# Kernel tuning notes

Hardware: AMD Instinct MI355X
Metric: run time of the kernel (lower is better)

## Reference

```python
import jax, jax.numpy as jnp
import numpy as np

ALPHA = 0.2   # leaky relu negative slope
EPS = 1e-5    # layernorm eps
NEG = -1e12   # mask value from original code


def gat_layer(x, adj, W, a):
    # x: [N, F_in], adj: [N, N] bool, W: [F_in, F_out], a: [2*F_out, 1]
    F_out = W.shape[1]
    Wh = x @ W                                  # [N, F_out]
    # a^T [Wh_i ; Wh_j] decomposes into f1_i + f2_j (same math as the
    # O(N^2 * 2F) concat in the torch code, without materializing it)
    f1 = Wh @ a[:F_out]                         # [N, 1]
    f2 = Wh @ a[F_out:]                         # [N, 1]
    e = jax.nn.leaky_relu(f1 + f2.T, negative_slope=ALPHA)  # [N, N]
    att = jnp.where(adj, e, NEG)
    att = jax.nn.softmax(att, axis=1)           # dropout p=0.0 -> no-op
    return att @ Wh                             # [N, F_out]


def layernorm(x, g, b):
    mu = jnp.mean(x, axis=-1, keepdims=True)
    var = jnp.var(x, axis=-1, keepdims=True)
    return (x - mu) * jax.lax.rsqrt(var + EPS) * g + b


def setup_inputs() -> dict:
    N, F = 8192, 128
    key = jax.random.key(0)
    ks = jax.random.split(key, 12)
    inp = {
        "input_hs": jax.random.normal(ks[0], (2, N, F), jnp.float32),
        "adjs": jax.random.uniform(ks[1], (2, N, N)) < 0.3,   # bool adjacency
        "MPNN_emb": jax.random.normal(ks[2], (N, F), jnp.float32),
        "query": jax.random.normal(ks[3], (1, F), jnp.float32),
        # learned params (xavier-ish scale)
        "W0": jax.random.normal(ks[4], (F, F), jnp.float32) * (1.414 / np.sqrt(F)),
        "a0": jax.random.normal(ks[5], (2 * F, 1), jnp.float32) * 0.1,
        "W1": jax.random.normal(ks[6], (F, F), jnp.float32) * (1.414 / np.sqrt(F)),
        "a1": jax.random.normal(ks[7], (2 * F, 1), jnp.float32) * 0.1,
        "ln_gamma": jnp.ones((F,), jnp.float32),
        "ln_beta": jnp.zeros((F,), jnp.float32),
        "res": jax.random.normal(ks[8], (1, 1), jnp.float32) * 0.5,
    }
    return inp


def reference(input_hs, adjs, MPNN_emb, query, W0, a0, W1, a1, ln_gamma, ln_beta, res):
    h0 = gat_layer(input_hs[0], adjs[0], W0, a0)   # [N, F]
    h1 = gat_layer(input_hs[1], adjs[1], W1, a1)   # [N, F]
    q = layernorm(query, ln_gamma, ln_beta)        # [1, F]
    w1 = q @ h0.T                                  # [1, N]
    w2 = q @ h1.T
    w3 = q @ MPNN_emb.T
    scores = jax.nn.softmax(jnp.concatenate([w1, w2, w3], axis=0), axis=0)  # [3, N]
    # diag_embed(s) @ H is just per-row scaling s[:, None] * H
    mix = (scores[0][:, None] * h0
           + scores[1][:, None] * h1
           + scores[2][:, None] * MPNN_emb)
    return res * mix + input_hs[0]
```

## Files before the change

kernel.cpp:

```cpp
#include <hip/hip_runtime.h>
#include <hip/hip_bf16.h>
#include <cstdint>


#define N 8192
#define F 128
#define JS 8

typedef __attribute__((ext_vector_type(8))) short short8;
typedef __attribute__((ext_vector_type(8))) unsigned short ushort8;
typedef __attribute__((ext_vector_type(4))) float floatx4;

__device__ inline unsigned int f2bf(float x) {
  unsigned int u = __float_as_uint(x);
  u += 0x7FFFu + ((u >> 16) & 1u);
  return u >> 16;
}


__global__ __launch_bounds__(128) void k1_wh(
    const float* __restrict__ X2, const float* __restrict__ W0,
    const float* __restrict__ W1, const float* __restrict__ a0,
    const float* __restrict__ a1, unsigned short* __restrict__ Whbt,
    float* __restrict__ f1g, float* __restrict__ f2g) {
  const int l  = blockIdx.y;
  const int i0 = blockIdx.x * 16;
  const int c  = threadIdx.x;
  const float* __restrict__ X = X2 + (size_t)l * N * F + (size_t)i0 * F;
  const float* __restrict__ W = l ? W1 : W0;

  __shared__ __align__(16) float sX[16 * F];
  __shared__ float red[2][2][16];
  {
    const float4* src = (const float4*)X;
    float4* dst = (float4*)sX;
#pragma unroll
    for (int qq = 0; qq < 4; ++qq) dst[qq * 128 + c] = src[qq * 128 + c];
  }
  __syncthreads();

  float acc[16];
#pragma unroll
  for (int r = 0; r < 16; ++r) acc[r] = 0.f;

  for (int f4 = 0; f4 < 32; ++f4) {
    float w0 = W[(f4 * 4 + 0) * F + c];
    float w1 = W[(f4 * 4 + 1) * F + c];
    float w2 = W[(f4 * 4 + 2) * F + c];
    float w3 = W[(f4 * 4 + 3) * F + c];
#pragma unroll
    for (int r = 0; r < 16; ++r) {
      float4 xv = *(const float4*)(&sX[r * F + f4 * 4]);
      acc[r] = fmaf(xv.x, w0, acc[r]);
      acc[r] = fmaf(xv.y, w1, acc[r]);
      acc[r] = fmaf(xv.z, w2, acc[r]);
      acc[r] = fmaf(xv.w, w3, acc[r]);
    }
  }

  {
    unsigned short* wdst = Whbt + (size_t)l * F * N + (size_t)c * N + i0;
    ushort8 u0, u1;
#pragma unroll
    for (int r = 0; r < 8; ++r) {
      u0[r] = (unsigned short)f2bf(acc[r]);
      u1[r] = (unsigned short)f2bf(acc[8 + r]);
    }
    *(ushort8*)wdst = u0;
    *(ushort8*)(wdst + 8) = u1;
  }

  const float* __restrict__ a = l ? a1 : a0;
  const float a1c = a[c], a2c = a[F + c];
  const int w = c >> 6, lane = c & 63;
#pragma unroll
  for (int r = 0; r < 16; ++r) {
    float s1 = acc[r] * a1c;
    float s2 = acc[r] * a2c;
#pragma unroll
    for (int off = 32; off; off >>= 1) {
      s1 += __shfl_down(s1, off);
      s2 += __shfl_down(s2, off);
    }
    if (lane == 0) {
      red[w][0][r] = s1;
      red[w][1][r] = s2;
    }
  }
  __syncthreads();
  if (c < 16)
    f1g[l * N + i0 + c] = red[0][0][c] + red[1][0][c];
  else if (c < 32)
    f2g[l * N + i0 + c - 16] = red[0][1][c - 16] + red[1][1][c - 16];
}

__global__ __launch_bounds__(128) void k3_qln(
    const float* __restrict__ query, const float* __restrict__ gamma,
    const float* __restrict__ beta, float* __restrict__ qln) {
  const int t = threadIdx.x;
  float v = query[t];
  float s = v, sq = v * v;
#pragma unroll
  for (int off = 32; off; off >>= 1) {
    s += __shfl_down(s, off);
    sq += __shfl_down(sq, off);
  }
  __shared__ float sb[4];
  if ((t & 63) == 0) {
    sb[t >> 6] = s;
    sb[2 + (t >> 6)] = sq;
  }
  __syncthreads();
  float S = sb[0] + sb[1], SQ = sb[2] + sb[3];
  float mu = S * (1.f / 128.f);
  float var = SQ * (1.f / 128.f) - mu * mu;
  qln[t] = (v - mu) * rsqrtf(var + 1e-5f) * gamma[t] + beta[t];
}

__device__ inline short8 make_pfrag(float f1v, const float4& fa,
                                    const float4& fb, const int4& a0,
                                    const int4& a1, float& Lacc) {
  float p0, p1, p2, p3, p4, p5, p6, p7, sc;
  sc = f1v + fa.x; sc = fmaxf(sc, 0.2f * sc); p0 = a0.x ? __expf(sc) : 0.f;
  sc = f1v + fa.y; sc = fmaxf(sc, 0.2f * sc); p1 = a0.y ? __expf(sc) : 0.f;
  sc = f1v + fa.z; sc = fmaxf(sc, 0.2f * sc); p2 = a0.z ? __expf(sc) : 0.f;
  sc = f1v + fa.w; sc = fmaxf(sc, 0.2f * sc); p3 = a0.w ? __expf(sc) : 0.f;
  sc = f1v + fb.x; sc = fmaxf(sc, 0.2f * sc); p4 = a1.x ? __expf(sc) : 0.f;
  sc = f1v + fb.y; sc = fmaxf(sc, 0.2f * sc); p5 = a1.y ? __expf(sc) : 0.f;
  sc = f1v + fb.z; sc = fmaxf(sc, 0.2f * sc); p6 = a1.z ? __expf(sc) : 0.f;
  sc = f1v + fb.w; sc = fmaxf(sc, 0.2f * sc); p7 = a1.w ? __expf(sc) : 0.f;
  Lacc += ((p0 + p1) + (p2 + p3)) + ((p4 + p5) + (p6 + p7));
  union { unsigned int u[4]; short8 s8; } r;
  r.u[0] = f2bf(p0) | (f2bf(p1) << 16);
  r.u[1] = f2bf(p2) | (f2bf(p3) << 16);
  r.u[2] = f2bf(p4) | (f2bf(p5) << 16);
  r.u[3] = f2bf(p6) | (f2bf(p7) << 16);
  return r.s8;
}

__global__ __launch_bounds__(256) void k2_attn(
    const unsigned short* __restrict__ Whbt, const float* __restrict__ f1g,
    const float* __restrict__ f2g, const int* __restrict__ adj,
    float* __restrict__ hpart, float* __restrict__ Lpart) {
  const int l  = blockIdx.y;
  const int s  = blockIdx.z;
  const int i0 = blockIdx.x * 128;
  const int t  = threadIdx.x;
  const int wave = t >> 6, lane = t & 63;
  const int lpos = lane & 15, halfk = lane >> 4;

  __shared__ __align__(16) unsigned short sB[128][136];

  const unsigned short* __restrict__ WhbL = Whbt + (size_t)l * F * N;
  const int* __restrict__ adjL = adj + (size_t)l * N * N;
  const float* __restrict__ f2L = f2g + l * N;

  const int rowA = i0 + wave * 32 + lpos;
  const float f1a = f1g[l * N + rowA];
  const float f1b = f1g[l * N + rowA + 16];
  const int* __restrict__ adjA = adjL + (size_t)rowA * N + halfk * 8;
  const int* __restrict__ adjB = adjA + (size_t)16 * N;
  const float* __restrict__ f2base = f2L + halfk * 8;

  const unsigned short* __restrict__ wsrc = WhbL + (size_t)(t >> 1) * N + (t & 1) * 8;
  unsigned short* __restrict__ sdst = &sB[t >> 1][(t & 1) * 8];

  floatx4 acc[2][8];
#pragma unroll
  for (int mt = 0; mt < 2; ++mt)
#pragma unroll
    for (int nt = 0; nt < 8; ++nt) acc[mt][nt] = (floatx4){0.f, 0.f, 0.f, 0.f};
  float Lacc0 = 0.f, Lacc1 = 0.f;

  const int jbeg = s * (N / JS);

  int4 ca0 = *(const int4*)(adjA + jbeg);
  int4 ca1 = *(const int4*)(adjA + jbeg + 4);
  int4 cb0 = *(const int4*)(adjB + jbeg);
  int4 cb1 = *(const int4*)(adjB + jbeg + 4);

  for (int st = 0; st < (N / JS) / 128; ++st) {
    const int jb = jbeg + st * 128;
    __syncthreads();
#pragma unroll
    for (int r = 0; r < 8; ++r)
      *(uint4*)(sdst + r * 16) = *(const uint4*)(wsrc + jb + r * 16);
    __syncthreads();

#pragma unroll
    for (int s4 = 0; s4 < 4; ++s4) {
      const int j0 = jb + s4 * 32;
      int jn = j0 + 32;
      if (jn >= jbeg + (N / JS)) jn = jbeg;
      int4 na0 = *(const int4*)(adjA + jn);
      int4 na1 = *(const int4*)(adjA + jn + 4);
      int4 nb0 = *(const int4*)(adjB + jn);
      int4 nb1 = *(const int4*)(adjB + jn + 4);
      float4 fa = *(const float4*)(f2base + j0);
      float4 fb = *(const float4*)(f2base + j0 + 4);

      short8 af0 = make_pfrag(f1a, fa, fb, ca0, ca1, Lacc0);
      short8 af1 = make_pfrag(f1b, fa, fb, cb0, cb1, Lacc1);

      const unsigned short* bp = &sB[lpos][s4 * 32 + halfk * 8];
#pragma unroll
      for (int nt = 0; nt < 8; ++nt) {
        short8 bf = *(const short8*)(bp + nt * 16 * 136);
        acc[0][nt] = __builtin_amdgcn_mfma_f32_16x16x32_bf16(af0, bf, acc[0][nt], 0, 0, 0);
        acc[1][nt] = __builtin_amdgcn_mfma_f32_16x16x32_bf16(af1, bf, acc[1][nt], 0, 0, 0);
      }
      ca0 = na0; ca1 = na1; cb0 = nb0; cb1 = nb1;
    }
  }

  const size_t obase = ((size_t)(l * JS + s) * N + i0) * F;
  const size_t lbase = (size_t)(l * JS + s) * N + i0;
#pragma unroll
  for (int mt = 0; mt < 2; ++mt) {
    const int rb = wave * 32 + mt * 16 + halfk * 4;
#pragma unroll
    for (int nt = 0; nt < 8; ++nt) {
#pragma unroll
      for (int reg = 0; reg < 4; ++reg)
        hpart[obase + (size_t)(rb + reg) * F + nt * 16 + lpos] = acc[mt][nt][reg];
    }
  }
  Lacc0 += __shfl_xor(Lacc0, 16);
  Lacc0 += __shfl_xor(Lacc0, 32);
  Lacc1 += __shfl_xor(Lacc1, 16);
  Lacc1 += __shfl_xor(Lacc1, 32);
  if (halfk == 0) {
    Lpart[lbase + wave * 32 + lpos] = Lacc0;
    Lpart[lbase + wave * 32 + 16 + lpos] = Lacc1;
  }
}

__global__ __launch_bounds__(256) void k4_mix(
    const float* __restrict__ hpart, const float* __restrict__ Lpart,
    const float* __restrict__ MPNN, const float* __restrict__ qln,
    const float* __restrict__ x0, const float* __restrict__ res,
    float* __restrict__ out) {
  const int row  = blockIdx.x * 4 + (threadIdx.x >> 6);
  const int lane = threadIdx.x & 63;
  const int c    = lane * 2;

  float h0x = 0.f, h0y = 0.f, h1x = 0.f, h1y = 0.f, L0 = 0.f, L1 = 0.f;
#pragma unroll
  for (int sx = 0; sx < JS; ++sx) {
    float2 v0 = *(const float2*)&hpart[((size_t)(0 * JS + sx) * N + row) * F + c];
    float2 v1 = *(const float2*)&hpart[((size_t)(1 * JS + sx) * N + row) * F + c];
    h0x += v0.x; h0y += v0.y;
    h1x += v1.x; h1y += v1.y;
    L0 += Lpart[(size_t)(0 * JS + sx) * N + row];
    L1 += Lpart[(size_t)(1 * JS + sx) * N + row];
  }
  const float i0v = 1.f / L0, i1v = 1.f / L1;
  h0x *= i0v; h0y *= i0v;
  h1x *= i1v; h1y *= i1v;

  float2 mv = *(const float2*)&MPNN[(size_t)row * F + c];
  float2 qv = *(const float2*)&qln[c];
  float w1 = qv.x * h0x + qv.y * h0y;
  float w2 = qv.x * h1x + qv.y * h1y;
  float w3 = qv.x * mv.x + qv.y * mv.y;
#pragma unroll
  for (int off = 1; off < 64; off <<= 1) {
    w1 += __shfl_xor(w1, off);
    w2 += __shfl_xor(w2, off);
    w3 += __shfl_xor(w3, off);
  }
  float m = fmaxf(w1, fmaxf(w2, w3));
  float e1 = __expf(w1 - m), e2 = __expf(w2 - m), e3 = __expf(w3 - m);
  float inv = res[0] / (e1 + e2 + e3);
  float2 xr = *(const float2*)&x0[(size_t)row * F + c];
  float2 o;
  o.x = (e1 * h0x + e2 * h1x + e3 * mv.x) * inv + xr.x;
  o.y = (e1 * h0y + e2 * h1y + e3 * mv.y) * inv + xr.y;
  *(float2*)&out[(size_t)row * F + c] = o;
}

extern "C" void kernel_launch(void* const* d_in, const int* in_sizes, int n_in,
                              void* d_out, int out_size, void* d_ws,
                              size_t ws_size, hipStream_t stream) {
  const float* x2    = (const float*)d_in[0];
  const int*   adj   = (const int*)d_in[1];
  const float* mpnn  = (const float*)d_in[2];
  const float* query = (const float*)d_in[3];
  const float* W0    = (const float*)d_in[4];
  const float* a0    = (const float*)d_in[5];
  const float* W1    = (const float*)d_in[6];
  const float* a1    = (const float*)d_in[7];
  const float* gamma = (const float*)d_in[8];
  const float* beta  = (const float*)d_in[9];
  const float* res   = (const float*)d_in[10];

  float* ws = (float*)d_ws;
  unsigned short* Whbt = (unsigned short*)ws;
  float* hpart = ws + 1048576;
  float* f1g   = ws + 17825792;
  float* f2g   = ws + 17842176;
  float* Lpart = ws + 17858560;
  float* qln   = ws + 17989632;
  float* out   = (float*)d_out;

  k1_wh<<<dim3(N / 16, 2), 128, 0, stream>>>(x2, W0, W1, a0, a1, Whbt, f1g, f2g);
  k3_qln<<<1, 128, 0, stream>>>(query, gamma, beta, qln);
  k2_attn<<<dim3(N / 128, 2, JS), 256, 0, stream>>>(Whbt, f1g, f2g, adj, hpart,
                                                    Lpart);
  k4_mix<<<N / 4, 256, 0, stream>>>(hpart, Lpart, mpnn, qln, x2, res, out);
}
```

Measured before the change: 816.5 us.

## Pre-pack adjacency into bitmasks and truncate bf16 conversion in attention kernel

Adds a streaming pre-pass kernel that packs the int32 adjacency matrix into 32-bit bitmasks. The attention kernel then reads one uint4 of mask bits per 128-column stage instead of prefetching int4 adjacency vectors for every 32-column step. The intent is to move the bulk adjacency read into a simple coalesced streaming kernel and shrink the load pressure and registers inside the MFMA loop. The cost is one extra launch plus a 16 MB mask written and read back. Separately, the float-to-bf16 conversion of the attention probabilities now truncates instead of rounding to nearest even, which saves ALU work but adds a small precision loss.

```diff
diff --git a/kernel.cpp b/kernel.cpp
--- a/kernel.cpp
+++ b/kernel.cpp
@@ -17,6 +17,22 @@
   return u >> 16;
 }
 
+
+__global__ __launch_bounds__(256) void k0_pack(const int* __restrict__ adj,
+                                               unsigned int* __restrict__ mask) {
+  const size_t gid = (size_t)blockIdx.x * 256 + threadIdx.x;
+  const int4* p = (const int4*)adj + gid * 8;
+  unsigned int m = 0;
+#pragma unroll
+  for (int q = 0; q < 8; ++q) {
+    int4 v = p[q];
+    m |= (v.x != 0) ? (1u << (q * 4 + 0)) : 0u;
+    m |= (v.y != 0) ? (1u << (q * 4 + 1)) : 0u;
+    m |= (v.z != 0) ? (1u << (q * 4 + 2)) : 0u;
+    m |= (v.w != 0) ? (1u << (q * 4 + 3)) : 0u;
+  }
+  mask[gid] = m;
+}
 
 __global__ __launch_bounds__(128) void k1_wh(
     const float* __restrict__ X2, const float* __restrict__ W0,
@@ -118,29 +134,29 @@
 }
 
 __device__ inline short8 make_pfrag(float f1v, const float4& fa,
-                                    const float4& fb, const int4& a0,
-                                    const int4& a1, float& Lacc) {
+                                    const float4& fb, unsigned int bits,
+                                    float& Lacc) {
   float p0, p1, p2, p3, p4, p5, p6, p7, sc;
-  sc = f1v + fa.x; sc = fmaxf(sc, 0.2f * sc); p0 = a0.x ? __expf(sc) : 0.f;
-  sc = f1v + fa.y; sc = fmaxf(sc, 0.2f * sc); p1 = a0.y ? __expf(sc) : 0.f;
-  sc = f1v + fa.z; sc = fmaxf(sc, 0.2f * sc); p2 = a0.z ? __expf(sc) : 0.f;
-  sc = f1v + fa.w; sc = fmaxf(sc, 0.2f * sc); p3 = a0.w ? __expf(sc) : 0.f;
-  sc = f1v + fb.x; sc = fmaxf(sc, 0.2f * sc); p4 = a1.x ? __expf(sc) : 0.f;
-  sc = f1v + fb.y; sc = fmaxf(sc, 0.2f * sc); p5 = a1.y ? __expf(sc) : 0.f;
-  sc = f1v + fb.z; sc = fmaxf(sc, 0.2f * sc); p6 = a1.z ? __expf(sc) : 0.f;
-  sc = f1v + fb.w; sc = fmaxf(sc, 0.2f * sc); p7 = a1.w ? __expf(sc) : 0.f;
+  sc = f1v + fa.x; sc = fmaxf(sc, 0.2f * sc); p0 = (bits & 1u)   ? __expf(sc) : 0.f;
+  sc = f1v + fa.y; sc = fmaxf(sc, 0.2f * sc); p1 = (bits & 2u)   ? __expf(sc) : 0.f;
+  sc = f1v + fa.z; sc = fmaxf(sc, 0.2f * sc); p2 = (bits & 4u)   ? __expf(sc) : 0.f;
+  sc = f1v + fa.w; sc = fmaxf(sc, 0.2f * sc); p3 = (bits & 8u)   ? __expf(sc) : 0.f;
+  sc = f1v + fb.x; sc = fmaxf(sc, 0.2f * sc); p4 = (bits & 16u)  ? __expf(sc) : 0.f;
+  sc = f1v + fb.y; sc = fmaxf(sc, 0.2f * sc); p5 = (bits & 32u)  ? __expf(sc) : 0.f;
+  sc = f1v + fb.z; sc = fmaxf(sc, 0.2f * sc); p6 = (bits & 64u)  ? __expf(sc) : 0.f;
+  sc = f1v + fb.w; sc = fmaxf(sc, 0.2f * sc); p7 = (bits & 128u) ? __expf(sc) : 0.f;
   Lacc += ((p0 + p1) + (p2 + p3)) + ((p4 + p5) + (p6 + p7));
   union { unsigned int u[4]; short8 s8; } r;
-  r.u[0] = f2bf(p0) | (f2bf(p1) << 16);
-  r.u[1] = f2bf(p2) | (f2bf(p3) << 16);
-  r.u[2] = f2bf(p4) | (f2bf(p5) << 16);
-  r.u[3] = f2bf(p6) | (f2bf(p7) << 16);
+  r.u[0] = (__float_as_uint(p0) >> 16) | (__float_as_uint(p1) & 0xFFFF0000u);
+  r.u[1] = (__float_as_uint(p2) >> 16) | (__float_as_uint(p3) & 0xFFFF0000u);
+  r.u[2] = (__float_as_uint(p4) >> 16) | (__float_as_uint(p5) & 0xFFFF0000u);
+  r.u[3] = (__float_as_uint(p6) >> 16) | (__float_as_uint(p7) & 0xFFFF0000u);
   return r.s8;
 }
 
 __global__ __launch_bounds__(256) void k2_attn(
     const unsigned short* __restrict__ Whbt, const float* __restrict__ f1g,
-    const float* __restrict__ f2g, const int* __restrict__ adj,
+    const float* __restrict__ f2g, const unsigned int* __restrict__ mask,
     float* __restrict__ hpart, float* __restrict__ Lpart) {
   const int l  = blockIdx.y;
   const int s  = blockIdx.z;
@@ -148,19 +164,19 @@
   const int t  = threadIdx.x;
   const int wave = t >> 6, lane = t & 63;
   const int lpos = lane & 15, halfk = lane >> 4;
+  const int shk = halfk * 8;
 
   __shared__ __align__(16) unsigned short sB[128][136];
 
   const unsigned short* __restrict__ WhbL = Whbt + (size_t)l * F * N;
-  const int* __restrict__ adjL = adj + (size_t)l * N * N;
   const float* __restrict__ f2L = f2g + l * N;
 
   const int rowA = i0 + wave * 32 + lpos;
   const float f1a = f1g[l * N + rowA];
   const float f1b = f1g[l * N + rowA + 16];
-  const int* __restrict__ adjA = adjL + (size_t)rowA * N + halfk * 8;
-  const int* __restrict__ adjB = adjA + (size_t)16 * N;
-  const float* __restrict__ f2base = f2L + halfk * 8;
+  const unsigned int* __restrict__ mrowA = mask + ((size_t)l * N + rowA) * (N / 32);
+  const unsigned int* __restrict__ mrowB = mrowA + 16 * (N / 32);
+  const float* __restrict__ f2base = f2L + shk;
 
   const unsigned short* __restrict__ wsrc = WhbL + (size_t)(t >> 1) * N + (t & 1) * 8;
   unsigned short* __restrict__ sdst = &sB[t >> 1][(t & 1) * 8];
@@ -174,13 +190,11 @@
 
   const int jbeg = s * (N / JS);
 
-  int4 ca0 = *(const int4*)(adjA + jbeg);
-  int4 ca1 = *(const int4*)(adjA + jbeg + 4);
-  int4 cb0 = *(const int4*)(adjB + jbeg);
-  int4 cb1 = *(const int4*)(adjB + jbeg + 4);
-
   for (int st = 0; st < (N / JS) / 128; ++st) {
     const int jb = jbeg + st * 128;
+    uint4 mwA = *(const uint4*)(mrowA + (jb >> 5));
+    uint4 mwB = *(const uint4*)(mrowB + (jb >> 5));
+
     __syncthreads();
 #pragma unroll
     for (int r = 0; r < 8; ++r)
@@ -190,26 +204,21 @@
 #pragma unroll
     for (int s4 = 0; s4 < 4; ++s4) {
       const int j0 = jb + s4 * 32;
-      int jn = j0 + 32;
-      if (jn >= jbeg + (N / JS)) jn = jbeg;
-      int4 na0 = *(const int4*)(adjA + jn);
-      int4 na1 = *(const int4*)(adjA + jn + 4);
-      int4 nb0 = *(const int4*)(adjB + jn);
-      int4 nb1 = *(const int4*)(adjB + jn + 4);
+      const unsigned int bitsA = (((const unsigned int*)&mwA)[s4] >> shk) & 0xFFu;
+      const unsigned int bitsB = (((const unsigned int*)&mwB)[s4] >> shk) & 0xFFu;
       float4 fa = *(const float4*)(f2base + j0);
       float4 fb = *(const float4*)(f2base + j0 + 4);
 
-      short8 af0 = make_pfrag(f1a, fa, fb, ca0, ca1, Lacc0);
-      short8 af1 = make_pfrag(f1b, fa, fb, cb0, cb1, Lacc1);
-
-      const unsigned short* bp = &sB[lpos][s4 * 32 + halfk * 8];
+      short8 af0 = make_pfrag(f1a, fa, fb, bitsA, Lacc0);
+      short8 af1 = make_pfrag(f1b, fa, fb, bitsB, Lacc1);
+
+      const unsigned short* bp = &sB[lpos][s4 * 32 + shk];
 #pragma unroll
       for (int nt = 0; nt < 8; ++nt) {
         short8 bf = *(const short8*)(bp + nt * 16 * 136);
         acc[0][nt] = __builtin_amdgcn_mfma_f32_16x16x32_bf16(af0, bf, acc[0][nt], 0, 0, 0);
         acc[1][nt] = __builtin_amdgcn_mfma_f32_16x16x32_bf16(af1, bf, acc[1][nt], 0, 0, 0);
       }
-      ca0 = na0; ca1 = na1; cb0 = nb0; cb1 = nb1;
     }
   }
 
@@ -296,16 +305,18 @@
 
   float* ws = (float*)d_ws;
   unsigned short* Whbt = (unsigned short*)ws;
-  float* hpart = ws + 1048576;
-  float* f1g   = ws + 17825792;
-  float* f2g   = ws + 17842176;
-  float* Lpart = ws + 17858560;
-  float* qln   = ws + 17989632;
+  unsigned int* maskb  = (unsigned int*)(ws + 1048576);
+  float* hpart = ws + 5242880;
+  float* f1g   = ws + 22020096;
+  float* f2g   = ws + 22036480;
+  float* Lpart = ws + 22052864;
+  float* qln   = ws + 22183936;
   float* out   = (float*)d_out;
 
+  k0_pack<<<2 * N * (N / 32) / 256, 256, 0, stream>>>(adj, maskb);
   k1_wh<<<dim3(N / 16, 2), 128, 0, stream>>>(x2, W0, W1, a0, a1, Whbt, f1g, f2g);
   k3_qln<<<1, 128, 0, stream>>>(query, gamma, beta, qln);
-  k2_attn<<<dim3(N / 128, 2, JS), 256, 0, stream>>>(Whbt, f1g, f2g, adj, hpart,
-                                                    Lpart);
+  k2_attn<<<dim3(N / 128, 2, JS), 256, 0, stream>>>(Whbt, f1g, f2g, maskb,
+                                                    hpart, Lpart);
   k4_mix<<<N / 4, 256, 0, stream>>>(hpart, Lpart, mpnn, qln, x2, res, out);
 }
```

Result: slower. 838.4 us (+2.7%).
